# Optimization experiments

Measured on AMD Instinct MI355X. Metric: run time of the kernel, lower is better.

The kernel has to match this reference:

```python
import jax, jax.numpy as jnp
import numpy as np

NP_, NB_, E_, BE_ = 10000, 30000, 300000, 8192
PIN, BIN, EA = 128, 128, 16
HID, GH = 64, 4
D, TH, L, NC, SEQ = 128, 4, 2, 10, 6


def _ln(x, g, b, eps=1e-5):
    m = x.mean(-1, keepdims=True)
    v = ((x - m) ** 2).mean(-1, keepdims=True)
    return (x - m) * jax.lax.rsqrt(v + eps) * g + b


def _seg_softmax(e, seg, n):
    m = jax.ops.segment_max(e, seg, num_segments=n)
    m = jnp.where(jnp.isfinite(m), m, 0.0)
    ex = jnp.exp(e - m[seg])
    s = jax.ops.segment_sum(ex, seg, num_segments=n)
    return ex / (s[seg] + 1e-16)


def _gatv2(xs, xd, es, ed, ea, Wl, bl, Wr, br, We, att, bias, n_dst):
    # PyG GATv2Conv, concat=False, add_self_loops=False, eval mode (no dropout)
    xl = (xs @ Wl + bl).reshape(-1, GH, HID)   # [Ns,H,C] source transform (message content)
    xr = (xd @ Wr + br).reshape(-1, GH, HID)   # [Nd,H,C] dest transform
    eh = (ea @ We).reshape(-1, GH, HID)        # [E,H,C] edge transform (no bias in PyG)
    msg = xl[es] + xr[ed] + eh                 # [E,H,C]
    score = jnp.einsum('ehc,hc->eh', jax.nn.leaky_relu(msg, 0.2), att)
    alpha = _seg_softmax(score, ed, n_dst)     # softmax over in-edges per dest node
    out = jax.ops.segment_sum(alpha[..., None] * xl[es], ed, num_segments=n_dst)
    return out.mean(axis=1) + bias             # concat=False -> mean over heads


def _mha(x, Wqkv, bqkv, Wo, bo):
    S, d = x.shape
    dh = d // TH
    q, k, v = jnp.split(x @ Wqkv + bqkv, 3, axis=-1)
    q = q.reshape(S, TH, dh).transpose(1, 0, 2)
    k = k.reshape(S, TH, dh).transpose(1, 0, 2)
    v = v.reshape(S, TH, dh).transpose(1, 0, 2)
    a = jax.nn.softmax(jnp.einsum('hqd,hkd->hqk', q, k) / jnp.sqrt(jnp.float32(dh)), axis=-1)
    o = jnp.einsum('hqk,hkd->hqd', a, v).transpose(1, 0, 2).reshape(S, d)
    return o @ Wo + bo


def _forward(pitcher_feat, batter_feat, edge_attr, history_states,
             Wp, bp, Wb, bb,
             rel_Wl, rel_bl, rel_Wr, rel_br, rel_We, rel_att, rel_bias,
             rev_Wl, rev_bl, rev_Wr, rev_br, rev_We, rev_att, rev_bias,
             Wgs, bgs, Wet, bet, pos,
             Wqkv, bqkv, Wo, bo, ln1g, ln1b, W1, b1, W2, b2, ln2g, ln2b,
             Wc1, bc1, Wc2, bc2,
             edge_src, edge_dst, edge_ids):
    gelu = lambda t: jax.nn.gelu(t, approximate=False)
    px = gelu(pitcher_feat @ Wp + bp)
    bx = gelu(batter_feat @ Wb + bb)
    # ('pitcher','faces','batter'): messages pitcher->batter, aggregated at batter nodes
    h_b = gelu(_gatv2(px, bx, edge_src, edge_dst, edge_attr,
                      rel_Wl, rel_bl, rel_Wr, rel_br, rel_We, rel_att, rel_bias, bx.shape[0]))
    # reversed relation: batter->pitcher, aggregated at pitcher nodes
    h_p = gelu(_gatv2(bx, px, edge_dst, edge_src, edge_attr,
                      rev_Wl, rev_bl, rev_Wr, rev_br, rev_We, rev_att, rev_bias, px.shape[0]))
    state = jnp.concatenate([h_p.mean(0), h_b.mean(0), edge_attr.mean(0)], -1) @ Wgs + bgs
    tok = jnp.concatenate([h_p[edge_src[edge_ids]], h_b[edge_dst[edge_ids]],
                           edge_attr[edge_ids]], -1) @ Wet + bet
    x = jnp.concatenate([history_states, state[None]], 0) + pos[:SEQ]
    for i in range(L):  # post-LN TransformerEncoderLayer, gelu activation, eval (no dropout)
        x = _ln(x + _mha(x, Wqkv[i], bqkv[i], Wo[i], bo[i]), ln1g[i], ln1b[i])
        f = gelu(x @ W1[i] + b1[i]) @ W2[i] + b2[i]
        x = _ln(x + f, ln2g[i], ln2b[i])
    ctx = x[-1]
    cat = jnp.concatenate([tok, jnp.broadcast_to(ctx, (tok.shape[0], D))], -1)
    return gelu(cat @ Wc1 + bc1) @ Wc2 + bc2


def setup_inputs() -> dict:
    key = jax.random.key(0)
    ks = iter(jax.random.split(key, 64))
    nrm = lambda shape, s: jax.random.normal(next(ks), shape, dtype=jnp.float32) * s
    d = {
        'pitcher_feat': nrm((NP_, PIN), 1.0),
        'batter_feat': nrm((NB_, BIN), 1.0),
        'edge_attr': nrm((E_, EA), 1.0),
        'history_states': nrm((SEQ - 1, D), 1.0),
        'Wp': nrm((PIN, HID), 0.05), 'bp': jnp.zeros((HID,), jnp.float32),
        'Wb': nrm((BIN, HID), 0.05), 'bb': jnp.zeros((HID,), jnp.float32),
    }
    for p in ('rel', 'rev'):
        d[p + '_Wl'] = nrm((HID, GH * HID), 0.05)
        d[p + '_bl'] = jnp.zeros((GH * HID,), jnp.float32)
        d[p + '_Wr'] = nrm((HID, GH * HID), 0.05)
        d[p + '_br'] = jnp.zeros((GH * HID,), jnp.float32)
        d[p + '_We'] = nrm((EA, GH * HID), 0.05)
        d[p + '_att'] = nrm((GH, HID), 0.05)
        d[p + '_bias'] = jnp.zeros((HID,), jnp.float32)
    cin = 2 * HID + EA
    d['Wgs'] = nrm((cin, D), 0.05); d['bgs'] = jnp.zeros((D,), jnp.float32)
    d['Wet'] = nrm((cin, D), 0.05); d['bet'] = jnp.zeros((D,), jnp.float32)
    d['pos'] = nrm((SEQ, D), 0.02)
    d['Wqkv'] = nrm((L, D, 3 * D), 0.05); d['bqkv'] = jnp.zeros((L, 3 * D), jnp.float32)
    d['Wo'] = nrm((L, D, D), 0.05); d['bo'] = jnp.zeros((L, D), jnp.float32)
    d['ln1g'] = jnp.ones((L, D), jnp.float32); d['ln1b'] = jnp.zeros((L, D), jnp.float32)
    d['W1'] = nrm((L, D, 4 * D), 0.05); d['b1'] = jnp.zeros((L, 4 * D), jnp.float32)
    d['W2'] = nrm((L, 4 * D, D), 0.05); d['b2'] = jnp.zeros((L, D), jnp.float32)
    d['ln2g'] = jnp.ones((L, D), jnp.float32); d['ln2b'] = jnp.zeros((L, D), jnp.float32)
    d['Wc1'] = nrm((2 * D, D), 0.05); d['bc1'] = jnp.zeros((D,), jnp.float32)
    d['Wc2'] = nrm((D, NC), 0.05); d['bc2'] = jnp.zeros((NC,), jnp.float32)
    d['edge_src'] = jax.random.randint(next(ks), (E_,), 0, NP_)
    d['edge_dst'] = jax.random.randint(next(ks), (E_,), 0, NB_)
    d['edge_ids'] = jax.random.randint(next(ks), (BE_,), 0, E_)
    return d


def reference(pitcher_feat, batter_feat, edge_attr, history_states,
              Wp, bp, Wb, bb,
              rel_Wl, rel_bl, rel_Wr, rel_br, rel_We, rel_att, rel_bias,
              rev_Wl, rev_bl, rev_Wr, rev_br, rev_We, rev_att, rev_bias,
              Wgs, bgs, Wet, bet, pos,
              Wqkv, bqkv, Wo, bo, ln1g, ln1b, W1, b1, W2, b2, ln2g, ln2b,
              Wc1, bc1, Wc2, bc2,
              edge_src, edge_dst, edge_ids):
    return _forward(pitcher_feat, batter_feat, edge_attr, history_states,
                    Wp, bp, Wb, bb,
                    rel_Wl, rel_bl, rel_Wr, rel_br, rel_We, rel_att, rel_bias,
                    rev_Wl, rev_bl, rev_Wr, rev_br, rev_We, rev_att, rev_bias,
                    Wgs, bgs, Wet, bet, pos,
                    Wqkv, bqkv, Wo, bo, ln1g, ln1b, W1, b1, W2, b2, ln2g, ln2b,
                    Wc1, bc1, Wc2, bc2,
                    edge_src, edge_dst, edge_ids)
```

## Files before the change

### kernel.cpp

```cpp
#include <hip/hip_runtime.h>
#include <math.h>

#define NP 10000
#define NB 30000
#define NEDGE 300000
#define BEDGE 8192
#define EAD 16
#define HID 64
#define GH 4
#define CW 256
#define DD 128
#define SEQ 6
#define NCLS 10
#define L 2
#define NEACOL 64

#if defined(__has_builtin)
#  if __has_builtin(__builtin_amdgcn_fdot2)
#    define HAVE_DOT2 1
#  else
#    define HAVE_DOT2 0
#  endif
#else
#  define HAVE_DOT2 0
#endif

typedef _Float16 h16x2 __attribute__((ext_vector_type(2)));

__device__ __forceinline__ float geluf(float x){
  return 0.5f * x * (1.0f + erff(x * 0.7071067811865475f));
}

__device__ __forceinline__ float b2f(unsigned short u){
  unsigned v = ((unsigned)u) << 16;
  return __int_as_float(v);
}
__device__ __forceinline__ unsigned short f2b(float f){
  unsigned x = __float_as_uint(f);
  unsigned r = x + 0x7FFF + ((x >> 16) & 1);
  return (unsigned short)(r >> 16);
}

typedef __attribute__((ext_vector_type(8))) short bf16x8;
typedef __attribute__((ext_vector_type(4))) float f32x4;

template<int KQ, int NTILES, bool A_F32, bool GELU>
__device__ __forceinline__
void mfma_gemm_body(int bid, const void* __restrict__ Av, const float* __restrict__ W,
                    const float* __restrict__ bias, unsigned short* __restrict__ out,
                    int M, unsigned short* __restrict__ sWt)
{
  constexpr int N  = NTILES * 16;
  constexpr int KP = KQ + 8;
  constexpr int NP8 = N + 8;
  int t = threadIdx.x, w = t >> 6, l = t & 63;
  int c = l & 15, g = l >> 4;
  for (int idx = t; idx < KQ*N; idx += 256){
    int k = idx / N, n = idx - k*N;
    sWt[n*KP + k] = f2b(W[idx]);
  }
  __syncthreads();
  int rowbase = bid*64 + w*16;
  int arow = rowbase + c; if (arow > M-1) arow = M-1;
  f32x4 acc[NTILES] = {};
  #pragma unroll
  for (int ks = 0; ks < KQ/32; ++ks){
    int koff = ks*32 + g*8;
    bf16x8 a;
    if constexpr (A_F32){
      const float* Af = (const float*)Av + (size_t)arow*KQ + koff;
      float4 f0 = *(const float4*)Af;
      float4 f1 = *(const float4*)(Af + 4);
      a[0]=(short)f2b(f0.x); a[1]=(short)f2b(f0.y); a[2]=(short)f2b(f0.z); a[3]=(short)f2b(f0.w);
      a[4]=(short)f2b(f1.x); a[5]=(short)f2b(f1.y); a[6]=(short)f2b(f1.z); a[7]=(short)f2b(f1.w);
    } else {
      a = *(const bf16x8*)((const unsigned short*)Av + (size_t)arow*KQ + koff);
    }
    #pragma unroll
    for (int nt = 0; nt < NTILES; ++nt){
      bf16x8 b = *(const bf16x8*)&sWt[(nt*16 + c)*KP + koff];
      acc[nt] = __builtin_amdgcn_mfma_f32_16x16x32_bf16(a, b, acc[nt], 0, 0, 0);
    }
  }
  __syncthreads();
  #pragma unroll
  for (int nt = 0; nt < NTILES; ++nt){
    #pragma unroll
    for (int j = 0; j < 4; ++j){
      float v = acc[nt][j] + bias[nt*16 + c];
      if (GELU) v = geluf(v);
      sWt[(w*16 + g*4 + j)*NP8 + nt*16 + c] = f2b(v);
    }
  }
  __syncthreads();
  int blockrow0 = bid*64;
  constexpr int C8 = N/8;
  for (int idx = t; idx < 64*C8; idx += 256){
    int row = idx / C8, c8 = idx - row*C8;
    if (blockrow0 + row < M){
      *(int4*)(out + (size_t)(blockrow0 + row)*N + c8*8) =
          *(const int4*)&sWt[row*NP8 + c8*8];
    }
  }
}

__global__ __launch_bounds__(256)
void k1_count_enc(const int* __restrict__ edst, const int* __restrict__ esrc,
                  int* __restrict__ degA, int* __restrict__ degB,
                  const float* __restrict__ pit, const float* __restrict__ Wp,
                  const float* __restrict__ bp, unsigned short* __restrict__ px,
                  const float* __restrict__ bat, const float* __restrict__ Wb,
                  const float* __restrict__ bb, unsigned short* __restrict__ bx,
                  int nbCount, int nbP)
{
  __shared__ unsigned short sWt[64*136];
  int b = blockIdx.x;
  if (b < nbCount){
    int i = b*256 + threadIdx.x;
    if (i < NEDGE){
      atomicAdd(&degA[edst[i]], 1);
      atomicAdd(&degB[esrc[i]], 1);
    }
  } else if (b < nbCount + nbP){
    mfma_gemm_body<128,4,true,true>(b - nbCount, pit, Wp, bp, px, NP, sWt);
  } else {
    mfma_gemm_body<128,4,true,true>(b - nbCount - nbP, bat, Wb, bb, bx, NB, sWt);
  }
}

__device__ void scan_dev(const int* __restrict__ deg, int* __restrict__ row_start,
                         int* __restrict__ cursor, int n){
  __shared__ int wsum[16];
  __shared__ int sbase;
  int t = threadIdx.x, w = t >> 6, l = t & 63;
  if (t == 0) sbase = 0;
  __syncthreads();
  for (int base = 0; base < n; base += 4096){
    int i = base + t*4;
    int4 v = make_int4(0,0,0,0);
    if (i < n) v = *(const int4*)(deg + i);
    int tsum = v.x + v.y + v.z + v.w;
    int x = tsum;
    #pragma unroll
    for (int off = 1; off < 64; off <<= 1){
      int y = __shfl_up(x, off);
      if (l >= off) x += y;
    }
    if (l == 63) wsum[w] = x;
    __syncthreads();
    int woff = 0, tot = 0;
    #pragma unroll
    for (int ww = 0; ww < 16; ++ww){
      int wv = wsum[ww];
      if (ww < w) woff += wv;
      tot += wv;
    }
    int excl = sbase + woff + x - tsum;
    if (i < n){
      int e1 = excl + v.x, e2 = excl + v.x + v.y, e3 = excl + v.x + v.y + v.z;
      row_start[i]   = excl; cursor[i]   = excl;
      row_start[i+1] = e1;   cursor[i+1] = e1;
      row_start[i+2] = e2;   cursor[i+2] = e2;
      row_start[i+3] = e3;   cursor[i+3] = e3;
    }
    __syncthreads();
    if (t == 0) sbase += tot;
    __syncthreads();
  }
  if (t == 0) row_start[n] = sbase;
}

__global__ __launch_bounds__(1024)
void scan2_kernel(const int* __restrict__ degA, int* __restrict__ rsA, int* __restrict__ curA, int nA,
                  const int* __restrict__ degB, int* __restrict__ rsB, int* __restrict__ curB, int nB,
                  float* __restrict__ mvec){
  if (blockIdx.x == 0){
    scan_dev(degA, rsA, curA, nA);
  } else {
    if (threadIdx.x < 144) mvec[threadIdx.x] = 0.f;
    scan_dev(degB, rsB, curB, nB);
  }
}

__global__ __launch_bounds__(256)
void k2_scatter_proj(const int* __restrict__ edst, const int* __restrict__ esrc,
                     int* __restrict__ curA, int* __restrict__ curB,
                     int2* __restrict__ csrA, int2* __restrict__ csrB,
                     const unsigned short* __restrict__ px, const unsigned short* __restrict__ bx,
                     const float* __restrict__ rel_Wl, const float* __restrict__ rel_bl,
                     const float* __restrict__ rel_Wr, const float* __restrict__ rel_br,
                     const float* __restrict__ rev_Wl, const float* __restrict__ rev_bl,
                     const float* __restrict__ rev_Wr, const float* __restrict__ rev_br,
                     unsigned short* __restrict__ xlA, unsigned short* __restrict__ xrA,
                     unsigned short* __restrict__ xlB, unsigned short* __restrict__ xrB,
                     int nbScat, int nbP, int nbB)
{
  __shared__ unsigned short sWt[256*72];
  int b = blockIdx.x;
  if (b < nbScat){
    int i = b*256 + threadIdx.x;
    if (i < NEDGE){
      int d = edst[i], s = esrc[i];
      int p = atomicAdd(&curA[d], 1);
      csrA[p] = make_int2(i, s);
      int q = atomicAdd(&curB[s], 1);
      csrB[q] = make_int2(i, d);
    }
  } else {
    b -= nbScat;
    if (b < nbP)               mfma_gemm_body<64,16,false,false>(b,            px, rel_Wl, rel_bl, xlA, NP, sWt);
    else if (b < nbP + nbB)    mfma_gemm_body<64,16,false,false>(b-nbP,        bx, rel_Wr, rel_br, xrA, NB, sWt);
    else if (b < nbP + 2*nbB)  mfma_gemm_body<64,16,false,false>(b-nbP-nbB,    bx, rev_Wl, rev_bl, xlB, NB, sWt);
    else                       mfma_gemm_body<64,16,false,false>(b-nbP-2*nbB,  px, rev_Wr, rev_br, xrB, NP, sWt);
  }
}

__device__ __forceinline__ void colsum_seg(int bid, int nb, const float4* __restrict__ in4,
                                           long total4, int n4, float* __restrict__ out,
                                           float scale, float* lds){
  int t = threadIdx.x, l = t & 63, w = t >> 6;
  long gid = (long)bid*256 + t;
  long stride = (long)nb*256;
  float4 acc = make_float4(0.f,0.f,0.f,0.f);
  for (long i = gid; i < total4; i += stride){
    float4 v = in4[i];
    acc.x += v.x; acc.y += v.y; acc.z += v.z; acc.w += v.w;
  }
  for (int off = n4; off < 64; off <<= 1){
    acc.x += __shfl_xor(acc.x, off);
    acc.y += __shfl_xor(acc.y, off);
    acc.z += __shfl_xor(acc.z, off);
    acc.w += __shfl_xor(acc.w, off);
  }
  if (l < n4) *(float4*)&lds[(w*n4 + l)*4] = acc;
  __syncthreads();
  if (t < n4*4){
    float sum = lds[t] + lds[n4*4 + t] + lds[2*n4*4 + t] + lds[3*n4*4 + t];
    atomicAdd(&out[t], sum * scale);
  }
  __syncthreads();
}

#if HAVE_DOT2
typedef int evt_t;
__device__ __forceinline__ int evload(const float* __restrict__ ea, int e, int l){
  float2 fv = *(const float2*)(ea + (size_t)e*EAD + 2*(l & 7));
  return __builtin_bit_cast(int, __builtin_amdgcn_cvt_pkrtz(fv.x, fv.y));
}
#define GAT_PAIR(X0, X1, EV0, EV1, V1OK, P0MASK)                             \
  {                                                                          \
    float x0 = b2f(X0.x), x1 = b2f(X0.y), x2 = b2f(X0.z), x3 = b2f(X0.w);    \
    float y0 = b2f(X1.x), y1 = b2f(X1.y), y2 = b2f(X1.z), y3 = b2f(X1.w);    \
    float h00 = x0 + r0, h01 = x1 + r1, h02 = x2 + r2, h03 = x3 + r3;        \
    float h10 = y0 + r0, h11 = y1 + r1, h12 = y2 + r2, h13 = y3 + r3;        \
    _Pragma("unroll")                                                        \
    for (int j = 0; j < 8; ++j){                                             \
      int c0 = __builtin_amdgcn_readlane(EV0, j);                            \
      int c1 = __builtin_amdgcn_readlane(EV1, j);                            \
      h16x2 e0 = __builtin_bit_cast(h16x2, c0);                              \
      h16x2 e1 = __builtin_bit_cast(h16x2, c1);                              \
      int4 wr = *(const int4*)&sWeH[j*CW + 4*l];                             \
      h16x2 w0 = __builtin_bit_cast(h16x2, wr.x);                            \
      h16x2 w1 = __builtin_bit_cast(h16x2, wr.y);                            \
      h16x2 w2 = __builtin_bit_cast(h16x2, wr.z);                            \
      h16x2 w3 = __builtin_bit_cast(h16x2, wr.w);                            \
      h00 = __builtin_amdgcn_fdot2(e0, w0, h00, false);                      \
      h01 = __builtin_amdgcn_fdot2(e0, w1, h01, false);                      \
      h02 = __builtin_amdgcn_fdot2(e0, w2, h02, false);                      \
      h03 = __builtin_amdgcn_fdot2(e0, w3, h03, false);                      \
      h10 = __builtin_amdgcn_fdot2(e1, w0, h10, false);                      \
      h11 = __builtin_amdgcn_fdot2(e1, w1, h11, false);                      \
      h12 = __builtin_amdgcn_fdot2(e1, w2, h12, false);                      \
      h13 = __builtin_amdgcn_fdot2(e1, w3, h13, false);                      \
    }                                                                        \
    h00 = fmaxf(h00, 0.2f*h00) * at.x;                                       \
    h01 = fmaxf(h01, 0.2f*h01) * at.y;                                       \
    h02 = fmaxf(h02, 0.2f*h02) * at.z;                                       \
    h03 = fmaxf(h03, 0.2f*h03) * at.w;                                       \
    h10 = fmaxf(h10, 0.2f*h10) * at.x;                                       \
    h11 = fmaxf(h11, 0.2f*h11) * at.y;                                       \
    h12 = fmaxf(h12, 0.2f*h12) * at.z;                                       \
    h13 = fmaxf(h13, 0.2f*h13) * at.w;                                       \
    float g0 = (h00 + h01) + (h02 + h03);                                    \
    float g1 = (h10 + h11) + (h12 + h13);                                    \
    _Pragma("unroll")                                                        \
    for (int off = 1; off < 16; off <<= 1){                                  \
      g0 += __shfl_xor(g0, off);                                             \
      g1 += __shfl_xor(g1, off);                                             \
    }                                                                        \
    float p0 = (P0MASK) ? __expf(g0) : 0.f;                                  \
    float p1 = (V1OK) ? __expf(g1) : 0.f;                                    \
    s += p0 + p1;                                                            \
    a0 = fmaf(p0, x0, fmaf(p1, y0, a0));                                     \
    a1 = fmaf(p0, x1, fmaf(p1, y1, a1));                                     \
    a2 = fmaf(p0, x2, fmaf(p1, y2, a2));                                     \
    a3 = fmaf(p0, x3, fmaf(p1, y3, a3));                                     \
  }
#else
typedef float evt_t;
__device__ __forceinline__ float evload(const float* __restrict__ ea, int e, int l){
  return ea[(size_t)e*EAD + (l & 15)];
}
#define GAT_PAIR(X0, X1, EV0, EV1, V1OK, P0MASK)                             \
  {                                                                          \
    float x0 = b2f(X0.x), x1 = b2f(X0.y), x2 = b2f(X0.z), x3 = b2f(X0.w);    \
    float y0 = b2f(X1.x), y1 = b2f(X1.y), y2 = b2f(X1.z), y3 = b2f(X1.w);    \
    float h00 = x0 + r0, h01 = x1 + r1, h02 = x2 + r2, h03 = x3 + r3;        \
    float h10 = y0 + r0, h11 = y1 + r1, h12 = y2 + r2, h13 = y3 + r3;        \
    int ia0 = __float_as_int(EV0);                                           \
    int ia1 = __float_as_int(EV1);                                           \
    _Pragma("unroll")                                                        \
    for (int k = 0; k < EAD; ++k){                                           \
      float c0 = __int_as_float(__builtin_amdgcn_readlane(ia0, k));          \
      float c1 = __int_as_float(__builtin_amdgcn_readlane(ia1, k));          \
      float4 wv = *(const float4*)&sWeH[k*CW + 4*l];                         \
      h00 = fmaf(c0, wv.x, h00); h01 = fmaf(c0, wv.y, h01);                  \
      h02 = fmaf(c0, wv.z, h02); h03 = fmaf(c0, wv.w, h03);                  \
      h10 = fmaf(c1, wv.x, h10); h11 = fmaf(c1, wv.y, h11);                  \
      h12 = fmaf(c1, wv.z, h12); h13 = fmaf(c1, wv.w, h13);                  \
    }                                                                        \
    h00 = fmaxf(h00, 0.2f*h00) * at.x;                                       \
    h01 = fmaxf(h01, 0.2f*h01) * at.y;                                       \
    h02 = fmaxf(h02, 0.2f*h02) * at.z;                                       \
    h03 = fmaxf(h03, 0.2f*h03) * at.w;                                       \
    h10 = fmaxf(h10, 0.2f*h10) * at.x;                                       \
    h11 = fmaxf(h11, 0.2f*h11) * at.y;                                       \
    h12 = fmaxf(h12, 0.2f*h12) * at.z;                                       \
    h13 = fmaxf(h13, 0.2f*h13) * at.w;                                       \
    float g0 = (h00 + h01) + (h02 + h03);                                    \
    float g1 = (h10 + h11) + (h12 + h13);                                    \
    _Pragma("unroll")                                                        \
    for (int off = 1; off < 16; off <<= 1){                                  \
      g0 += __shfl_xor(g0, off);                                             \
      g1 += __shfl_xor(g1, off);                                             \
    }                                                                        \
    float p0 = (P0MASK) ? __expf(g0) : 0.f;                                  \
    float p1 = (V1OK) ? __expf(g1) : 0.f;                                    \
    s += p0 + p1;                                                            \
    a0 = fmaf(p0, x0, fmaf(p1, y0, a0));                                     \
    a1 = fmaf(p0, x1, fmaf(p1, y1, a1));                                     \
    a2 = fmaf(p0, x2, fmaf(p1, y2, a2));                                     \
    a3 = fmaf(p0, x3, fmaf(p1, y3, a3));                                     \
  }
#endif

__global__ __launch_bounds__(256)
void gat2_kernel(const unsigned short* __restrict__ xlA_, const unsigned short* __restrict__ xrA_,
                 const float* __restrict__ WeA, const float* __restrict__ attA,
                 const float* __restrict__ biasA, const int2* __restrict__ csrA_,
                 const int* __restrict__ rsA_, float* __restrict__ houtA,
                 const unsigned short* __restrict__ xlB_, const unsigned short* __restrict__ xrB_,
                 const float* __restrict__ WeB, const float* __restrict__ attB,
                 const float* __restrict__ biasB, const int2* __restrict__ csrB_,
                 const int* __restrict__ rsB_, float* __restrict__ houtB,
                 const float* __restrict__ ea, float* __restrict__ mvec, int gsplit)
{
#if HAVE_DOT2
  __shared__ int sWeH[8*CW];
#else
  __shared__ float sWeH[16*CW];
#endif
  __shared__ float csum[4][16][4];
  int t = threadIdx.x, l = t & 63;
  int b = blockIdx.x;
  if (b < NEACOL){
    colsum_seg(b, NEACOL, (const float4*)ea, (long)NEDGE*EAD/4, 4,
               mvec + 128, 1.f/NEDGE, &csum[0][0][0]);
    return;
  }
  b -= NEACOL;
  int ngat = (int)gridDim.x - NEACOL;
  bool isA = b < gsplit;
  const unsigned short* xl = isA ? xlA_ : xlB_;
  const unsigned short* xr = isA ? xrA_ : xrB_;
  const float* We   = isA ? WeA   : WeB;
  const float* att  = isA ? attA  : attB;
  const float* bias = isA ? biasA : biasB;
  const int2* csr   = isA ? csrA_ : csrB_;
  const int* row_start = isA ? rsA_ : rsB_;
  float* hout = isA ? houtA : houtB;
  int ndst = isA ? NB : NP;
  int bid  = isA ? b : b - gsplit;
  int nblk = isA ? gsplit : ngat - gsplit;

#if HAVE_DOT2
  for (int i = t; i < 8*CW; i += 256){
    int j = i >> 8, c = i & 255;
    sWeH[i] = __builtin_bit_cast(int,
        __builtin_amdgcn_cvt_pkrtz(We[(2*j)*CW + c], We[(2*j+1)*CW + c]));
  }
#else
  for (int i = t*4; i < 16*CW; i += 1024)
    *(float4*)&sWeH[i] = *(const float4*)&We[i];
#endif
  __syncthreads();
  float4 at = *(const float4*)&att[4*l];
  float4 bi = *(const float4*)&bias[(l & 15)*4];
  float cs0 = 0.f, cs1 = 0.f, cs2 = 0.f, cs3 = 0.f;
  int wid = bid*4 + (t >> 6);
  int nw = nblk*4;
  for (int d = wid; d < ndst; d += nw){
    ushort4 ru = *(const ushort4*)(xr + (size_t)d*CW + 4*l);
    float r0 = b2f(ru.x), r1 = b2f(ru.y), r2 = b2f(ru.z), r3 = b2f(ru.w);
    int rs = row_start[d], re = row_start[d+1];
    float s = 0.f;
    float a0 = 0.f, a1 = 0.f, a2 = 0.f, a3 = 0.f;
    if (rs < re){
      int last = re - 1;
      #define CLMP(x) ((x) > last ? last : (x))
      int2 qA0 = csr[rs],         qA1 = csr[CLMP(rs+1)];
      int2 qB0 = csr[CLMP(rs+2)], qB1 = csr[CLMP(rs+3)];
      int2 nA0 = csr[CLMP(rs+4)], nA1 = csr[CLMP(rs+5)];
      int2 nB0 = csr[CLMP(rs+6)], nB1 = csr[CLMP(rs+7)];
      ushort4 xA0 = *(const ushort4*)(xl + (size_t)qA0.y*CW + 4*l);
      ushort4 xA1 = *(const ushort4*)(xl + (size_t)qA1.y*CW + 4*l);
      evt_t  evA0 = evload(ea, qA0.x, l);
      evt_t  evA1 = evload(ea, qA1.x, l);
      ushort4 xB0 = *(const ushort4*)(xl + (size_t)qB0.y*CW + 4*l);
      ushort4 xB1 = *(const ushort4*)(xl + (size_t)qB1.y*CW + 4*l);
      evt_t  evB0 = evload(ea, qB0.x, l);
      evt_t  evB1 = evload(ea, qB1.x, l);
      for (int i = rs; i < re; i += 4){
        int2 mA0 = csr[CLMP(i+8)],  mA1 = csr[CLMP(i+9)];
        int2 mB0 = csr[CLMP(i+10)], mB1 = csr[CLMP(i+11)];
        GAT_PAIR(xA0, xA1, evA0, evA1, (i+1 < re), true);
        xA0 = *(const ushort4*)(xl + (size_t)nA0.y*CW + 4*l);
        xA1 = *(const ushort4*)(xl + (size_t)nA1.y*CW + 4*l);
        evA0 = evload(ea, nA0.x, l);
        evA1 = evload(ea, nA1.x, l);
        nA0 = mA0; nA1 = mA1;
        GAT_PAIR(xB0, xB1, evB0, evB1, (i+3 < re), (i+2 < re));
        xB0 = *(const ushort4*)(xl + (size_t)nB0.y*CW + 4*l);
        xB1 = *(const ushort4*)(xl + (size_t)nB1.y*CW + 4*l);
        evB0 = evload(ea, nB0.x, l);
        evB1 = evload(ea, nB1.x, l);
        nB0 = mB0; nB1 = mB1;
      }
      #undef CLMP
    }
    float inv = 1.f / (s + 1e-16f);
    float v0 = a0*inv, v1 = a1*inv, v2 = a2*inv, v3 = a3*inv;
    v0 += __shfl_xor(v0, 16); v1 += __shfl_xor(v1, 16);
    v2 += __shfl_xor(v2, 16); v3 += __shfl_xor(v3, 16);
    v0 += __shfl_xor(v0, 32); v1 += __shfl_xor(v1, 32);
    v2 += __shfl_xor(v2, 32); v3 += __shfl_xor(v3, 32);
    if (l < 16){
      float4 o;
      o.x = geluf(v0*0.25f + bi.x);
      o.y = geluf(v1*0.25f + bi.y);
      o.z = geluf(v2*0.25f + bi.z);
      o.w = geluf(v3*0.25f + bi.w);
      *(float4*)(hout + (size_t)d*HID + 4*l) = o;
      cs0 += o.x; cs1 += o.y; cs2 += o.z; cs3 += o.w;
    }
  }
  int w = t >> 6;
  if (l < 16){
    csum[w][l][0] = cs0; csum[w][l][1] = cs1;
    csum[w][l][2] = cs2; csum[w][l][3] = cs3;
  }
  __syncthreads();
  if (t < 64){
    int lq = t >> 2, j = t & 3;
    float sum = csum[0][lq][j] + csum[1][lq][j] + csum[2][lq][j] + csum[3][lq][j];
    float scale = isA ? (1.f/NB) : (1.f/NP);
    float* dst = isA ? (mvec + 64) : mvec;
    atomicAdd(&dst[t], sum * scale);
  }
}

__device__ void gemmcat_body(int bid, const float* __restrict__ hp, const float* __restrict__ hb,
                             const float* __restrict__ ea, const int* __restrict__ esrc,
                             const int* __restrict__ edst, const int* __restrict__ eids,
                             const float* __restrict__ W, const float* __restrict__ bias,
                             float* __restrict__ out)
{
  __shared__ float sAT[16][68];
  __shared__ float sB[16][68];
  __shared__ int sS[64], sD[64], sE[64];
  int t = threadIdx.x;
  int m0 = (bid >> 1)*64, n0 = (bid & 1)*64;
  if (t < 64){
    int e = eids[m0 + t];
    sS[t] = esrc[e]; sD[t] = edst[e]; sE[t] = e;
  }
  __syncthreads();
  int tr = t >> 4, tc = t & 15;
  float acc[4][4] = {};
  for (int k0 = 0; k0 < 144; k0 += 16){
    {
      int r = t >> 2, c = (t & 3) * 4;
      const float* src; int col = k0 + c;
      if (k0 < 64)       { src = hp + (size_t)sS[r]*HID; }
      else if (k0 < 128) { src = hb + (size_t)sD[r]*HID; col -= 64; }
      else               { src = ea + (size_t)sE[r]*EAD; col -= 128; }
      float4 va = *(const float4*)(src + col);
      sAT[c+0][r] = va.x; sAT[c+1][r] = va.y; sAT[c+2][r] = va.z; sAT[c+3][r] = va.w;
    }
    {
      int r = t >> 4, c = (t & 15) * 4;
      float4 vb = *(const float4*)(W + (size_t)(k0+r)*DD + n0 + c);
      *(float4*)&sB[r][c] = vb;
    }
    __syncthreads();
    #pragma unroll
    for (int k = 0; k < 16; ++k){
      float4 av = *(const float4*)&sAT[k][tr*4];
      float4 bv = *(const float4*)&sB[k][tc*4];
      acc[0][0] = fmaf(av.x, bv.x, acc[0][0]);
      acc[0][1] = fmaf(av.x, bv.y, acc[0][1]);
      acc[0][2] = fmaf(av.x, bv.z, acc[0][2]);
      acc[0][3] = fmaf(av.x, bv.w, acc[0][3]);
      acc[1][0] = fmaf(av.y, bv.x, acc[1][0]);
      acc[1][1] = fmaf(av.y, bv.y, acc[1][1]);
      acc[1][2] = fmaf(av.y, bv.z, acc[1][2]);
      acc[1][3] = fmaf(av.y, bv.w, acc[1][3]);
      acc[2][0] = fmaf(av.z, bv.x, acc[2][0]);
      acc[2][1] = fmaf(av.z, bv.y, acc[2][1]);
      acc[2][2] = fmaf(av.z, bv.z, acc[2][2]);
      acc[2][3] = fmaf(av.z, bv.w, acc[2][3]);
      acc[3][0] = fmaf(av.w, bv.x, acc[3][0]);
      acc[3][1] = fmaf(av.w, bv.y, acc[3][1]);
      acc[3][2] = fmaf(av.w, bv.z, acc[3][2]);
      acc[3][3] = fmaf(av.w, bv.w, acc[3][3]);
    }
    __syncthreads();
  }
  #pragma unroll
  for (int i = 0; i < 4; ++i){
    int gr = m0 + tr*4 + i;
    float4 v;
    v.x = acc[i][0] + bias[n0 + tc*4 + 0];
    v.y = acc[i][1] + bias[n0 + tc*4 + 1];
    v.z = acc[i][2] + bias[n0 + tc*4 + 2];
    v.w = acc[i][3] + bias[n0 + tc*4 + 3];
    *(float4*)(out + (size_t)gr*DD + n0 + tc*4) = v;
  }
}

__global__ __launch_bounds__(256)
void gemmcat_kernel(const float* __restrict__ hp, const float* __restrict__ hb,
                    const float* __restrict__ ea, const int* __restrict__ esrc,
                    const int* __restrict__ edst, const int* __restrict__ eids,
                    const float* __restrict__ Wet, const float* __restrict__ bet,
                    float* __restrict__ tokb)
{
  gemmcat_body(blockIdx.x, hp, hb, ea, esrc, edst, eids, Wet, bet, tokb);
}

template<int K, int N, int NC>
__device__ __forceinline__ void qstageF(const float* __restrict__ x,
                                        const float* __restrict__ W,
                                        float (&a)[6][4], int q, int ch)
{
  constexpr int NQ = N/4;
  constexpr int KC = K/NC;
  constexpr int J  = KC/4;
  const float4* wp = (const float4*)W + (size_t)(ch*KC)*NQ + q;
  const float* xb = x + ch*KC;
  float4 wv[KC];
  int kx[J];
  #pragma unroll
  for (int j = 0; j < J; ++j){
    int k4 = (j + ch) & (J-1);
    kx[j] = k4;
    wv[j*4+0] = wp[(size_t)(k4*4+0)*NQ];
    wv[j*4+1] = wp[(size_t)(k4*4+1)*NQ];
    wv[j*4+2] = wp[(size_t)(k4*4+2)*NQ];
    wv[j*4+3] = wp[(size_t)(k4*4+3)*NQ];
  }
  #pragma unroll
  for (int s = 0; s < 6; ++s){ a[s][0]=0.f; a[s][1]=0.f; a[s][2]=0.f; a[s][3]=0.f; }
  #pragma unroll
  for (int j = 0; j < J; ++j){
    #pragma unroll
    for (int s = 0; s < 6; ++s){
      float4 xv = *(const float4*)&xb[s*K + kx[j]*4];
      a[s][0]=fmaf(xv.x,wv[j*4+0].x,a[s][0]); a[s][0]=fmaf(xv.y,wv[j*4+1].x,a[s][0]);
      a[s][0]=fmaf(xv.z,wv[j*4+2].x,a[s][0]); a[s][0]=fmaf(xv.w,wv[j*4+3].x,a[s][0]);
      a[s][1]=fmaf(xv.x,wv[j*4+0].y,a[s][1]); a[s][1]=fmaf(xv.y,wv[j*4+1].y,a[s][1]);
      a[s][1]=fmaf(xv.z,wv[j*4+2].y,a[s][1]); a[s][1]=fmaf(xv.w,wv[j*4+3].y,a[s][1]);
      a[s][2]=fmaf(xv.x,wv[j*4+0].z,a[s][2]); a[s][2]=fmaf(xv.y,wv[j*4+1].z,a[s][2]);
      a[s][2]=fmaf(xv.z,wv[j*4+2].z,a[s][2]); a[s][2]=fmaf(xv.w,wv[j*4+3].z,a[s][2]);
      a[s][3]=fmaf(xv.x,wv[j*4+0].w,a[s][3]); a[s][3]=fmaf(xv.y,wv[j*4+1].w,a[s][3]);
      a[s][3]=fmaf(xv.z,wv[j*4+2].w,a[s][3]); a[s][3]=fmaf(xv.w,wv[j*4+3].w,a[s][3]);
    }
  }
  #pragma unroll
  for (int off = 1; off < NC; off <<= 1){
    #pragma unroll
    for (int s = 0; s < 6; ++s){
      a[s][0]+=__shfl_xor(a[s][0],off); a[s][1]+=__shfl_xor(a[s][1],off);
      a[s][2]+=__shfl_xor(a[s][2],off); a[s][3]+=__shfl_xor(a[s][3],off);
    }
  }
}

__global__ __launch_bounds__(512)
void xform_kernel(const float* __restrict__ hist, const float* __restrict__ mvec,
                  const float* __restrict__ Wgs, const float* __restrict__ bgs,
                  const float* __restrict__ pos,
                  const float* __restrict__ Wqkv, const float* __restrict__ bqkv,
                  const float* __restrict__ Wo, const float* __restrict__ bo,
                  const float* __restrict__ ln1g, const float* __restrict__ ln1b,
                  const float* __restrict__ W1, const float* __restrict__ b1,
                  const float* __restrict__ W2, const float* __restrict__ b2,
                  const float* __restrict__ ln2g, const float* __restrict__ ln2b,
                  const float* __restrict__ Wc1, const float* __restrict__ bc1,
                  float* __restrict__ bias2)
{
  __shared__ float sx[SEQ*DD];
  __shared__ float sq[SEQ*3*DD];
  __shared__ float sh[SEQ*512];
  __shared__ float st[SEQ*DD];
  __shared__ float sc[4][6][6];
  __shared__ float smv[144];
  int t = threadIdx.x;

  for (int i = t; i < (SEQ-1)*DD; i += 512) sx[i] = hist[i] + pos[i];
  if (t < 144) smv[t] = mvec[t];
  __syncthreads();
  if (t < 256){
    int q = t >> 3, ch = t & 7;
    float4 wv[18];
    #pragma unroll
    for (int kk = 0; kk < 18; ++kk)
      wv[kk] = *(const float4*)&Wgs[(ch*18+kk)*DD + q*4];
    float a0=0.f,a1=0.f,a2=0.f,a3=0.f;
    #pragma unroll
    for (int kk = 0; kk < 18; ++kk){
      float xv = smv[ch*18+kk];
      a0=fmaf(xv,wv[kk].x,a0); a1=fmaf(xv,wv[kk].y,a1);
      a2=fmaf(xv,wv[kk].z,a2); a3=fmaf(xv,wv[kk].w,a3);
    }
    #pragma unroll
    for (int off = 1; off < 8; off <<= 1){
      a0+=__shfl_xor(a0,off); a1+=__shfl_xor(a1,off);
      a2+=__shfl_xor(a2,off); a3+=__shfl_xor(a3,off);
    }
    if (ch == 0){
      int n = q*4, base = (SEQ-1)*DD + n;
      sx[base+0]=a0+bgs[n+0]+pos[base+0];
      sx[base+1]=a1+bgs[n+1]+pos[base+1];
      sx[base+2]=a2+bgs[n+2]+pos[base+2];
      sx[base+3]=a3+bgs[n+3]+pos[base+3];
    }
  }
  __syncthreads();

  for (int lyr = 0; lyr < L; ++lyr){
    if (t < 384){
      int q = t >> 2, ch = t & 3;
      const float* wq = Wqkv + (size_t)lyr*DD*3*DD;
      const float* bq = bqkv + lyr*3*DD;
      float a[6][4];
      qstageF<128,384,4>(sx, wq, a, q, ch);
      if (ch == 0){
        int n = q*4;
        #pragma unroll
        for (int s = 0; s < 6; ++s){
          sq[s*384+n+0]=a[s][0]+bq[n+0];
          sq[s*384+n+1]=a[s][1]+bq[n+1];
          sq[s*384+n+2]=a[s][2]+bq[n+2];
          sq[s*384+n+3]=a[s][3]+bq[n+3];
        }
      }
    }
    __syncthreads();
    if (t < 144){
      int h = t/36, r = t%36, qi = r/6, ki = r%6;
      float acc = 0.f;
      #pragma unroll
      for (int d2 = 0; d2 < 32; ++d2)
        acc = fmaf(sq[qi*384 + h*32 + d2], sq[ki*384 + 128 + h*32 + d2], acc);
      sc[h][qi][ki] = acc * 0.17677669529663687f;
    }
    __syncthreads();
    if (t < 24){
      int h = t/6, qi = t%6;
      float* row = sc[h][qi];
      float mx = row[0];
      #pragma unroll
      for (int k = 1; k < 6; ++k) mx = fmaxf(mx, row[k]);
      float sm = 0.f;
      #pragma unroll
      for (int k = 0; k < 6; ++k){ row[k] = __expf(row[k]-mx); sm += row[k]; }
      float inv = 1.f/sm;
      #pragma unroll
      for (int k = 0; k < 6; ++k) row[k] *= inv;
    }
    __syncthreads();
    for (int i = t; i < SEQ*DD; i += 512){
      int s = i >> 7, n = i & 127, h = n >> 5, d2 = n & 31;
      float acc = 0.f;
      #pragma unroll
      for (int ki = 0; ki < 6; ++ki)
        acc = fmaf(sc[h][s][ki], sq[ki*384 + 256 + h*32 + d2], acc);
      st[i] = acc;
    }
    __syncthreads();
    {
      int q = t >> 4, ch = t & 15;
      float a[6][4];
      qstageF<128,128,16>(st, Wo + (size_t)lyr*DD*DD, a, q, ch);
      if (ch == 0){
        int n = q*4;
        const float* bop = bo + lyr*DD;
        #pragma unroll
        for (int s = 0; s < 6; ++s){
          sh[s*128+n+0]=a[s][0]+bop[n+0]+sx[s*128+n+0];
          sh[s*128+n+1]=a[s][1]+bop[n+1]+sx[s*128+n+1];
          sh[s*128+n+2]=a[s][2]+bop[n+2]+sx[s*128+n+2];
          sh[s*128+n+3]=a[s][3]+bop[n+3]+sx[s*128+n+3];
        }
      }
    }
    __syncthreads();
    {
      int w = t >> 6, lw = t & 63;
      if (w < SEQ){
        const float* g = ln1g + lyr*DD; const float* be = ln1b + lyr*DD;
        float v0 = sh[w*DD + lw], v1 = sh[w*DD + 64 + lw];
        float sm = v0 + v1;
        #pragma unroll
        for (int off = 1; off < 64; off <<= 1) sm += __shfl_xor(sm, off);
        float mean = sm * 0.0078125f;
        float d0 = v0-mean, d1 = v1-mean;
        float qv = d0*d0 + d1*d1;
        #pragma unroll
        for (int off = 1; off < 64; off <<= 1) qv += __shfl_xor(qv, off);
        float inv = rsqrtf(qv*0.0078125f + 1e-5f);
        sx[w*DD + lw]      = d0*inv*g[lw] + be[lw];
        sx[w*DD + 64 + lw] = d1*inv*g[64+lw] + be[64+lw];
      }
    }
    __syncthreads();
    {
      int q = t >> 2, ch = t & 3;
      const float* w1 = W1 + (size_t)lyr*DD*512;
      const float* b1p = b1 + lyr*512;
      float a[6][4];
      qstageF<128,512,4>(sx, w1, a, q, ch);
      if (ch == 0){
        int n = q*4;
        #pragma unroll
        for (int s = 0; s < 6; ++s){
          sh[s*512+n+0]=geluf(a[s][0]+b1p[n+0]);
          sh[s*512+n+1]=geluf(a[s][1]+b1p[n+1]);
          sh[s*512+n+2]=geluf(a[s][2]+b1p[n+2]);
          sh[s*512+n+3]=geluf(a[s][3]+b1p[n+3]);
        }
      }
    }
    __syncthreads();
    {
      int q = t >> 4, ch = t & 15;
      const float* w2 = W2 + (size_t)lyr*512*DD;
      const float* b2p = b2 + lyr*DD;
      float a[6][4];
      qstageF<512,128,16>(sh, w2, a, q, ch);
      if (ch == 0){
        int n = q*4;
        #pragma unroll
        for (int s = 0; s < 6; ++s){
          st[s*128+n+0]=a[s][0]+b2p[n+0]+sx[s*128+n+0];
          st[s*128+n+1]=a[s][1]+b2p[n+1]+sx[s*128+n+1];
          st[s*128+n+2]=a[s][2]+b2p[n+2]+sx[s*128+n+2];
          st[s*128+n+3]=a[s][3]+b2p[n+3]+sx[s*128+n+3];
        }
      }
    }
    __syncthreads();
    {
      int w = t >> 6, lw = t & 63;
      if (w < SEQ){
        const float* g = ln2g + lyr*DD; const float* be = ln2b + lyr*DD;
        float v0 = st[w*DD + lw], v1 = st[w*DD + 64 + lw];
        float sm = v0 + v1;
        #pragma unroll
        for (int off = 1; off < 64; off <<= 1) sm += __shfl_xor(sm, off);
        float mean = sm * 0.0078125f;
        float d0 = v0-mean, d1 = v1-mean;
        float qv = d0*d0 + d1*d1;
        #pragma unroll
        for (int off = 1; off < 64; off <<= 1) qv += __shfl_xor(qv, off);
        float inv = rsqrtf(qv*0.0078125f + 1e-5f);
        sx[w*DD + lw]      = d0*inv*g[lw] + be[lw];
        sx[w*DD + 64 + lw] = d1*inv*g[64+lw] + be[64+lw];
      }
    }
    __syncthreads();
  }
  if (t < 256){
    int q = t >> 3, ch = t & 7;
    const float4* wp = (const float4*)(Wc1 + (size_t)DD*DD) + (size_t)(ch*16)*32 + q;
    const float* xb = &sx[(SEQ-1)*DD + ch*16];
    float4 wv[16];
    int kx[4];
    #pragma unroll
    for (int j = 0; j < 4; ++j){
      int k4 = (j + ch) & 3;
      kx[j] = k4;
      wv[j*4+0] = wp[(size_t)(k4*4+0)*32];
      wv[j*4+1] = wp[(size_t)(k4*4+1)*32];
      wv[j*4+2] = wp[(size_t)(k4*4+2)*32];
      wv[j*4+3] = wp[(size_t)(k4*4+3)*32];
    }
    float a0=0.f,a1=0.f,a2=0.f,a3=0.f;
    #pragma unroll
    for (int j = 0; j < 4; ++j){
      float4 xv = *(const float4*)&xb[kx[j]*4];
      a0=fmaf(xv.x,wv[j*4+0].x,a0); a0=fmaf(xv.y,wv[j*4+1].x,a0);
      a0=fmaf(xv.z,wv[j*4+2].x,a0); a0=fmaf(xv.w,wv[j*4+3].x,a0);
      a1=fmaf(xv.x,wv[j*4+0].y,a1); a1=fmaf(xv.y,wv[j*4+1].y,a1);
      a1=fmaf(xv.z,wv[j*4+2].y,a1); a1=fmaf(xv.w,wv[j*4+3].y,a1);
      a2=fmaf(xv.x,wv[j*4+0].z,a2); a2=fmaf(xv.y,wv[j*4+1].z,a2);
      a2=fmaf(xv.z,wv[j*4+2].z,a2); a2=fmaf(xv.w,wv[j*4+3].z,a2);
      a3=fmaf(xv.x,wv[j*4+0].w,a3); a3=fmaf(xv.y,wv[j*4+1].w,a3);
      a3=fmaf(xv.z,wv[j*4+2].w,a3); a3=fmaf(xv.w,wv[j*4+3].w,a3);
    }
    #pragma unroll
    for (int off = 1; off < 8; off <<= 1){
      a0+=__shfl_xor(a0,off); a1+=__shfl_xor(a1,off);
      a2+=__shfl_xor(a2,off); a3+=__shfl_xor(a3,off);
    }
    if (ch == 0){
      int n = q*4;
      bias2[n+0]=a0+bc1[n+0];
      bias2[n+1]=a1+bc1[n+1];
      bias2[n+2]=a2+bc1[n+2];
      bias2[n+3]=a3+bc1[n+3];
    }
  }
}

__global__ __launch_bounds__(256)
void cls_kernel(const float* __restrict__ A, const float* __restrict__ W,
                const float* __restrict__ bias2, const float* __restrict__ Wc2,
                const float* __restrict__ bc2, float* __restrict__ out)
{
  __shared__ float sAT[16][68];
  __shared__ float sB[16][132];
  __shared__ float sH[64][129];
  int t = threadIdx.x;
  int m0 = blockIdx.x * 64;
  int tr = t >> 4, tc = t & 15;
  float acc[4][8] = {};
  for (int k0 = 0; k0 < DD; k0 += 16){
    {
      int r = t >> 2, c = (t & 3) * 4;
      float4 va = *(const float4*)(A + (size_t)(m0+r)*DD + k0 + c);
      sAT[c+0][r] = va.x; sAT[c+1][r] = va.y; sAT[c+2][r] = va.z; sAT[c+3][r] = va.w;
    }
    {
      int r = t >> 4, c = (t & 15) * 8;
      float4 b0 = *(const float4*)(W + (size_t)(k0+r)*DD + c);
      float4 b1 = *(const float4*)(W + (size_t)(k0+r)*DD + c + 4);
      *(float4*)&sB[r][c] = b0;
      *(float4*)&sB[r][c+4] = b1;
    }
    __syncthreads();
    #pragma unroll
    for (int k = 0; k < 16; ++k){
      float4 av = *(const float4*)&sAT[k][tr*4];
      float4 b0 = *(const float4*)&sB[k][tc*8];
      float4 b1 = *(const float4*)&sB[k][tc*8+4];
      #pragma unroll
      for (int i = 0; i < 4; ++i){
        float avi = (i==0)?av.x:(i==1)?av.y:(i==2)?av.z:av.w;
        acc[i][0] = fmaf(avi, b0.x, acc[i][0]);
        acc[i][1] = fmaf(avi, b0.y, acc[i][1]);
        acc[i][2] = fmaf(avi, b0.z, acc[i][2]);
        acc[i][3] = fmaf(avi, b0.w, acc[i][3]);
        acc[i][4] = fmaf(avi, b1.x, acc[i][4]);
        acc[i][5] = fmaf(avi, b1.y, acc[i][5]);
        acc[i][6] = fmaf(avi, b1.z, acc[i][6]);
        acc[i][7] = fmaf(avi, b1.w, acc[i][7]);
      }
    }
    __syncthreads();
  }
  #pragma unroll
  for (int i = 0; i < 4; ++i){
    #pragma unroll
    for (int j = 0; j < 8; ++j){
      sH[tr*4+i][tc*8+j] = geluf(acc[i][j] + bias2[tc*8+j]);
    }
  }
  __syncthreads();
  if (t < 64){
    float a10[NCLS];
    #pragma unroll
    for (int c = 0; c < NCLS; ++c) a10[c] = bc2[c];
    for (int k = 0; k < DD; ++k){
      float hv = sH[t][k];
      #pragma unroll
      for (int c = 0; c < NCLS; ++c)
        a10[c] = fmaf(hv, Wc2[k*NCLS + c], a10[c]);
    }
    #pragma unroll
    for (int c = 0; c < NCLS; ++c)
      out[(size_t)(m0+t)*NCLS + c] = a10[c];
  }
}

extern "C" void kernel_launch(void* const* d_in, const int* in_sizes, int n_in,
                              void* d_out, int out_size, void* d_ws, size_t ws_size,
                              hipStream_t stream){
  (void)in_sizes; (void)n_in; (void)out_size; (void)ws_size;
  const float* pitcher = (const float*)d_in[0];
  const float* batter  = (const float*)d_in[1];
  const float* eattr   = (const float*)d_in[2];
  const float* hist    = (const float*)d_in[3];
  const float* Wp = (const float*)d_in[4];
  const float* bp = (const float*)d_in[5];
  const float* Wb = (const float*)d_in[6];
  const float* bb = (const float*)d_in[7];
  const float* rel_Wl  = (const float*)d_in[8];
  const float* rel_bl  = (const float*)d_in[9];
  const float* rel_Wr  = (const float*)d_in[10];
  const float* rel_br  = (const float*)d_in[11];
  const float* rel_We  = (const float*)d_in[12];
  const float* rel_att = (const float*)d_in[13];
  const float* rel_bias= (const float*)d_in[14];
  const float* rev_Wl  = (const float*)d_in[15];
  const float* rev_bl  = (const float*)d_in[16];
  const float* rev_Wr  = (const float*)d_in[17];
  const float* rev_br  = (const float*)d_in[18];
  const float* rev_We  = (const float*)d_in[19];
  const float* rev_att = (const float*)d_in[20];
  const float* rev_bias= (const float*)d_in[21];
  const float* Wgs = (const float*)d_in[22];
  const float* bgs = (const float*)d_in[23];
  const float* Wet = (const float*)d_in[24];
  const float* bet = (const float*)d_in[25];
  const float* pos = (const float*)d_in[26];
  const float* Wqkv= (const float*)d_in[27];
  const float* bqkv= (const float*)d_in[28];
  const float* Wo  = (const float*)d_in[29];
  const float* bo  = (const float*)d_in[30];
  const float* ln1g= (const float*)d_in[31];
  const float* ln1b= (const float*)d_in[32];
  const float* W1  = (const float*)d_in[33];
  const float* b1  = (const float*)d_in[34];
  const float* W2  = (const float*)d_in[35];
  const float* b2  = (const float*)d_in[36];
  const float* ln2g= (const float*)d_in[37];
  const float* ln2b= (const float*)d_in[38];
  const float* Wc1 = (const float*)d_in[39];
  const float* bc1 = (const float*)d_in[40];
  const float* Wc2 = (const float*)d_in[41];
  const float* bc2 = (const float*)d_in[42];
  const int* esrc = (const int*)d_in[43];
  const int* edst = (const int*)d_in[44];
  const int* eids = (const int*)d_in[45];

  char* w = (char*)d_ws;
  size_t off = 0;
  auto alloc = [&](size_t bytes)->void*{
    void* p = (void*)(w + off);
    off += (bytes + 255) & ~(size_t)255;
    return p;
  };
  unsigned short* px_bf  = (unsigned short*)alloc((size_t)NP*HID*2);
  unsigned short* bx_bf  = (unsigned short*)alloc((size_t)NB*HID*2);
  float*          hp     = (float*)alloc((size_t)NP*HID*4);
  float*          hb     = (float*)alloc((size_t)NB*HID*4);
  unsigned short* xlA    = (unsigned short*)alloc((size_t)NP*CW*2);
  unsigned short* xrA    = (unsigned short*)alloc((size_t)NB*CW*2);
  unsigned short* xlB    = (unsigned short*)alloc((size_t)NB*CW*2);
  unsigned short* xrB    = (unsigned short*)alloc((size_t)NP*CW*2);
  int*            degAB  = (int*)alloc((size_t)(NB+NP)*4);
  int*            degA   = degAB;
  int*            degB   = degAB + NB;
  int*            rowstA = (int*)alloc((size_t)(NB+1)*4);
  int*            rowstB = (int*)alloc((size_t)(NP+1)*4);
  int*            cursA  = (int*)alloc((size_t)NB*4);
  int*            cursB  = (int*)alloc((size_t)NP*4);
  int2*           csrA   = (int2*)alloc((size_t)NEDGE*8);
  int2*           csrB   = (int2*)alloc((size_t)NEDGE*8);
  float*          mvec   = (float*)alloc(144*4);
  float*          bias2  = (float*)alloc(DD*4);
  float*          tokb   = (float*)xlA;

  const int nbCount = (NEDGE + 255)/256;
  const int nbP = (NP + 63)/64;
  const int nbB = (NB + 63)/64;

  hipMemsetAsync(degAB, 0, (size_t)(NB+NP)*4, stream);
  k1_count_enc<<<nbCount + nbP + nbB, 256, 0, stream>>>(
      edst, esrc, degA, degB,
      pitcher, Wp, bp, px_bf, batter, Wb, bb, bx_bf, nbCount, nbP);

  scan2_kernel<<<2, 1024, 0, stream>>>(degA, rowstA, cursA, NB,
                                       degB, rowstB, cursB, NP, mvec);

  k2_scatter_proj<<<nbCount + 2*nbP + 2*nbB, 256, 0, stream>>>(
      edst, esrc, cursA, cursB, csrA, csrB, px_bf, bx_bf,
      rel_Wl, rel_bl, rel_Wr, rel_br, rev_Wl, rev_bl, rev_Wr, rev_br,
      xlA, xrA, xlB, xrB, nbCount, nbP, nbB);

  gat2_kernel<<<NEACOL + 4096, 256, 0, stream>>>(
      xlA, xrA, rel_We, rel_att, rel_bias, csrA, rowstA, hb,
      xlB, xrB, rev_We, rev_att, rev_bias, csrB, rowstB, hp,
      eattr, mvec, 2048);

  gemmcat_kernel<<<256, 256, 0, stream>>>(
      hp, hb, eattr, esrc, edst, eids, Wet, bet, tokb);

  xform_kernel<<<1, 512, 0, stream>>>(
      hist, mvec, Wgs, bgs, pos, Wqkv, bqkv, Wo, bo, ln1g, ln1b,
      W1, b1, W2, b2, ln2g, ln2b, Wc1, bc1, bias2);

  cls_kernel<<<BEDGE/64, 256, 0, stream>>>(tokb, Wc1, bias2, Wc2, bc2, (float*)d_out);
}
```

Measured before the change: 376.1 us.

## Merge gemmcat and transformer kernels into one launch; keep GAT weights in registers

Folds the single-block transformer (xform) kernel into the gemmcat launch as an extra block, so the two independent stages run at the same time and one kernel launch plus its serialization is removed. The xform body is rewritten for 256 threads using strided loops, which roughly doubles its per-thread serial work. The GAT edge kernel now preloads its eight packed-half We rows into registers once, instead of reading them from LDS for every edge pair. The register copy raises register pressure in the GAT kernel and may lower occupancy.

```diff
diff --git a/kernel.cpp b/kernel.cpp
--- a/kernel.cpp
+++ b/kernel.cpp
@@ -259,7 +259,7 @@
       int c1 = __builtin_amdgcn_readlane(EV1, j);                            \
       h16x2 e0 = __builtin_bit_cast(h16x2, c0);                              \
       h16x2 e1 = __builtin_bit_cast(h16x2, c1);                              \
-      int4 wr = *(const int4*)&sWeH[j*CW + 4*l];                             \
+      int4 wr = wreg[j];                                                     \
       h16x2 w0 = __builtin_bit_cast(h16x2, wr.x);                            \
       h16x2 w1 = __builtin_bit_cast(h16x2, wr.y);                            \
       h16x2 w2 = __builtin_bit_cast(h16x2, wr.z);                            \
@@ -394,6 +394,11 @@
     *(float4*)&sWeH[i] = *(const float4*)&We[i];
 #endif
   __syncthreads();
+#if HAVE_DOT2
+  int4 wreg[8];
+  #pragma unroll
+  for (int j = 0; j < 8; ++j) wreg[j] = *(const int4*)&sWeH[j*CW + 4*l];
+#endif
   float4 at = *(const float4*)&att[4*l];
   float4 bi = *(const float4*)&bias[(l & 15)*4];
   float cs0 = 0.f, cs1 = 0.f, cs2 = 0.f, cs3 = 0.f;
@@ -538,16 +543,6 @@
   }
 }
 
-__global__ __launch_bounds__(256)
-void gemmcat_kernel(const float* __restrict__ hp, const float* __restrict__ hb,
-                    const float* __restrict__ ea, const int* __restrict__ esrc,
-                    const int* __restrict__ edst, const int* __restrict__ eids,
-                    const float* __restrict__ Wet, const float* __restrict__ bet,
-                    float* __restrict__ tokb)
-{
-  gemmcat_body(blockIdx.x, hp, hb, ea, esrc, edst, eids, Wet, bet, tokb);
-}
-
 template<int K, int N, int NC>
 __device__ __forceinline__ void qstageF(const float* __restrict__ x,
                                         const float* __restrict__ W,
@@ -596,18 +591,17 @@
   }
 }
 
-__global__ __launch_bounds__(512)
-void xform_kernel(const float* __restrict__ hist, const float* __restrict__ mvec,
-                  const float* __restrict__ Wgs, const float* __restrict__ bgs,
-                  const float* __restrict__ pos,
-                  const float* __restrict__ Wqkv, const float* __restrict__ bqkv,
-                  const float* __restrict__ Wo, const float* __restrict__ bo,
-                  const float* __restrict__ ln1g, const float* __restrict__ ln1b,
-                  const float* __restrict__ W1, const float* __restrict__ b1,
-                  const float* __restrict__ W2, const float* __restrict__ b2,
-                  const float* __restrict__ ln2g, const float* __restrict__ ln2b,
-                  const float* __restrict__ Wc1, const float* __restrict__ bc1,
-                  float* __restrict__ bias2)
+__device__ void xform_body(const float* __restrict__ hist, const float* __restrict__ mvec,
+                           const float* __restrict__ Wgs, const float* __restrict__ bgs,
+                           const float* __restrict__ pos,
+                           const float* __restrict__ Wqkv, const float* __restrict__ bqkv,
+                           const float* __restrict__ Wo, const float* __restrict__ bo,
+                           const float* __restrict__ ln1g, const float* __restrict__ ln1b,
+                           const float* __restrict__ W1, const float* __restrict__ b1,
+                           const float* __restrict__ W2, const float* __restrict__ b2,
+                           const float* __restrict__ ln2g, const float* __restrict__ ln2b,
+                           const float* __restrict__ Wc1, const float* __restrict__ bc1,
+                           float* __restrict__ bias2)
 {
   __shared__ float sx[SEQ*DD];
   __shared__ float sq[SEQ*3*DD];
@@ -617,10 +611,10 @@
   __shared__ float smv[144];
   int t = threadIdx.x;
 
-  for (int i = t; i < (SEQ-1)*DD; i += 512) sx[i] = hist[i] + pos[i];
+  for (int i = t; i < (SEQ-1)*DD; i += 256) sx[i] = hist[i] + pos[i];
   if (t < 144) smv[t] = mvec[t];
   __syncthreads();
-  if (t < 256){
+  {
     int q = t >> 3, ch = t & 7;
     float4 wv[18];
     #pragma unroll
@@ -649,8 +643,8 @@
   __syncthreads();
 
   for (int lyr = 0; lyr < L; ++lyr){
-    if (t < 384){
-      int q = t >> 2, ch = t & 3;
+    for (int u = t; u < 384; u += 256){
+      int q = u >> 2, ch = u & 3;
       const float* wq = Wqkv + (size_t)lyr*DD*3*DD;
       const float* bq = bqkv + lyr*3*DD;
       float a[6][4];
@@ -690,7 +684,7 @@
       for (int k = 0; k < 6; ++k) row[k] *= inv;
     }
     __syncthreads();
-    for (int i = t; i < SEQ*DD; i += 512){
+    for (int i = t; i < SEQ*DD; i += 256){
       int s = i >> 7, n = i & 127, h = n >> 5, d2 = n & 31;
       float acc = 0.f;
       #pragma unroll
@@ -699,8 +693,8 @@
       st[i] = acc;
     }
     __syncthreads();
-    {
-      int q = t >> 4, ch = t & 15;
+    for (int u = t; u < 512; u += 256){
+      int q = u >> 4, ch = u & 15;
       float a[6][4];
       qstageF<128,128,16>(st, Wo + (size_t)lyr*DD*DD, a, q, ch);
       if (ch == 0){
@@ -717,10 +711,10 @@
     }
     __syncthreads();
     {
-      int w = t >> 6, lw = t & 63;
-      if (w < SEQ){
-        const float* g = ln1g + lyr*DD; const float* be = ln1b + lyr*DD;
-        float v0 = sh[w*DD + lw], v1 = sh[w*DD + 64 + lw];
+      int lw = t & 63;
+      const float* g = ln1g + lyr*DD; const float* be = ln1b + lyr*DD;
+      for (int row = (t >> 6); row < SEQ; row += 4){
+        float v0 = sh[row*DD + lw], v1 = sh[row*DD + 64 + lw];
         float sm = v0 + v1;
         #pragma unroll
         for (int off = 1; off < 64; off <<= 1) sm += __shfl_xor(sm, off);
@@ -730,13 +724,13 @@
         #pragma unroll
         for (int off = 1; off < 64; off <<= 1) qv += __shfl_xor(qv, off);
         float inv = rsqrtf(qv*0.0078125f + 1e-5f);
-        sx[w*DD + lw]      = d0*inv*g[lw] + be[lw];
-        sx[w*DD + 64 + lw] = d1*inv*g[64+lw] + be[64+lw];
+        sx[row*DD + lw]      = d0*inv*g[lw] + be[lw];
+        sx[row*DD + 64 + lw] = d1*inv*g[64+lw] + be[64+lw];
       }
     }
     __syncthreads();
-    {
-      int q = t >> 2, ch = t & 3;
+    for (int u = t; u < 512; u += 256){
+      int q = u >> 2, ch = u & 3;
       const float* w1 = W1 + (size_t)lyr*DD*512;
       const float* b1p = b1 + lyr*512;
       float a[6][4];
@@ -753,8 +747,8 @@
       }
     }
     __syncthreads();
-    {
-      int q = t >> 4, ch = t & 15;
+    for (int u = t; u < 512; u += 256){
+      int q = u >> 4, ch = u & 15;
       const float* w2 = W2 + (size_t)lyr*512*DD;
       const float* b2p = b2 + lyr*DD;
       float a[6][4];
@@ -772,10 +766,10 @@
     }
     __syncthreads();
     {
-      int w = t >> 6, lw = t & 63;
-      if (w < SEQ){
-        const float* g = ln2g + lyr*DD; const float* be = ln2b + lyr*DD;
-        float v0 = st[w*DD + lw], v1 = st[w*DD + 64 + lw];
+      int lw = t & 63;
+      const float* g = ln2g + lyr*DD; const float* be = ln2b + lyr*DD;
+      for (int row = (t >> 6); row < SEQ; row += 4){
+        float v0 = st[row*DD + lw], v1 = st[row*DD + 64 + lw];
         float sm = v0 + v1;
         #pragma unroll
         for (int off = 1; off < 64; off <<= 1) sm += __shfl_xor(sm, off);
@@ -785,13 +779,13 @@
         #pragma unroll
         for (int off = 1; off < 64; off <<= 1) qv += __shfl_xor(qv, off);
         float inv = rsqrtf(qv*0.0078125f + 1e-5f);
-        sx[w*DD + lw]      = d0*inv*g[lw] + be[lw];
-        sx[w*DD + 64 + lw] = d1*inv*g[64+lw] + be[64+lw];
+        sx[row*DD + lw]      = d0*inv*g[lw] + be[lw];
+        sx[row*DD + 64 + lw] = d1*inv*g[64+lw] + be[64+lw];
       }
     }
     __syncthreads();
   }
-  if (t < 256){
+  {
     int q = t >> 3, ch = t & 7;
     const float4* wp = (const float4*)(Wc1 + (size_t)DD*DD) + (size_t)(ch*16)*32 + q;
     const float* xb = &sx[(SEQ-1)*DD + ch*16];
@@ -831,6 +825,32 @@
       bias2[n+2]=a2+bc1[n+2];
       bias2[n+3]=a3+bc1[n+3];
     }
+  }
+}
+
+__global__ __launch_bounds__(256)
+void k3_gemmcat_xform(const float* __restrict__ hp, const float* __restrict__ hb,
+                      const float* __restrict__ ea, const int* __restrict__ esrc,
+                      const int* __restrict__ edst, const int* __restrict__ eids,
+                      const float* __restrict__ Wet, const float* __restrict__ bet,
+                      float* __restrict__ tokb,
+                      const float* __restrict__ hist, const float* __restrict__ mvec,
+                      const float* __restrict__ Wgs, const float* __restrict__ bgs,
+                      const float* __restrict__ pos,
+                      const float* __restrict__ Wqkv, const float* __restrict__ bqkv,
+                      const float* __restrict__ Wo, const float* __restrict__ bo,
+                      const float* __restrict__ ln1g, const float* __restrict__ ln1b,
+                      const float* __restrict__ W1, const float* __restrict__ b1,
+                      const float* __restrict__ W2, const float* __restrict__ b2,
+                      const float* __restrict__ ln2g, const float* __restrict__ ln2b,
+                      const float* __restrict__ Wc1, const float* __restrict__ bc1,
+                      float* __restrict__ bias2)
+{
+  if (blockIdx.x < 256){
+    gemmcat_body(blockIdx.x, hp, hb, ea, esrc, edst, eids, Wet, bet, tokb);
+  } else {
+    xform_body(hist, mvec, Wgs, bgs, pos, Wqkv, bqkv, Wo, bo, ln1g, ln1b,
+               W1, b1, W2, b2, ln2g, ln2b, Wc1, bc1, bias2);
   }
 }
 
@@ -1005,10 +1025,8 @@
       xlB, xrB, rev_We, rev_att, rev_bias, csrB, rowstB, hp,
       eattr, mvec, 2048);
 
-  gemmcat_kernel<<<256, 256, 0, stream>>>(
-      hp, hb, eattr, esrc, edst, eids, Wet, bet, tokb);
-
-  xform_kernel<<<1, 512, 0, stream>>>(
+  k3_gemmcat_xform<<<257, 256, 0, stream>>>(
+      hp, hb, eattr, esrc, edst, eids, Wet, bet, tokb,
       hist, mvec, Wgs, bgs, pos, Wqkv, bqkv, Wo, bo, ln1g, ln1b,
       W1, b1, W2, b2, ln2g, ln2b, Wc1, bc1, bias2);
 
```

New measurement: 416.2 us. 1.11x slower.
